# Optimization experiments

Measured on AMD Instinct MI355X. Metric: run time of the kernel, lower is better.

## Reference

```python
import jax, jax.numpy as jnp
import numpy as np

IN, OUT, HID = 1024, 1024, 2048
L = IN + OUT + HID
EPS = 1e-12  # F.normalize default eps


def _make_strength_matrix():
    fwd_s, bwd_s, lat_s, self_s = 1.0, 0.5, 0.3, 0.0
    i = np.arange(L)
    # torch: triu (incl diag) = forward, then tril (incl diag) = backward -> diag ends up backward here
    A = np.where(i[:, None] >= i[None, :], bwd_s, fwd_s).astype(np.float32)
    # lateral blocks (within input, within output, within hidden)
    A[0:IN, 0:IN] = lat_s
    A[IN:IN + OUT, IN:IN + OUT] = lat_s
    A[IN + OUT:L, IN + OUT:L] = lat_s
    A[i, i] = self_s
    return A


def setup_inputs() -> dict:
    key = jax.random.key(0)
    kx, ky, kw = jax.random.split(key, 3)
    B = 1024
    x = jax.random.normal(kx, (B, IN), dtype=jnp.float32)
    y = jax.random.normal(ky, (B, OUT), dtype=jnp.float32)
    W = jax.random.normal(kw, (L, L), dtype=jnp.float32) * 0.01
    idx = jnp.arange(L)
    W = W.at[idx, idx].set(0.0)  # fill_diagonal_(0) at init
    A = jnp.asarray(_make_strength_matrix())
    return {"x": x, "y": y, "W": W, "A": A, "n": 32}


def reference(x, y, W, A, n):
    # clamp_x=True, clamp_y=False, norm_hidden=True, average_window<=0
    B = x.shape[0]
    act0 = jnp.concatenate(
        [x, jnp.zeros_like(y), jnp.zeros((B, HID), dtype=x.dtype)], axis=1
    )  # [B, L]
    mw = W * A.T  # modified weights, loop-invariant

    def step(act, _):
        act = jax.nn.relu(act @ mw.T)          # linear(act, mw) + relu
        act = act.at[:, :IN].set(x)            # clamp_x
        hid = act[:, IN + OUT:]
        nrm = jnp.linalg.norm(hid, axis=1, keepdims=True)
        hid = hid / jnp.maximum(nrm, EPS)      # F.normalize p=2 dim=1
        act = act.at[:, IN + OUT:].set(hid)
        return act, None

    act, _ = jax.lax.scan(step, act0, None, length=n)
    return act
```

## Files before the change

kernel.cpp:

```cpp
#include <hip/hip_runtime.h>
#include <stdint.h>
#include <stddef.h>


#define L 4096
#define INX 1024
#define OUTX 1024
#define BATCH 1024
#define NCOL 3072
#define NITER 32

#define BM 128
#define BN 96
#define BK 64
#define SMEM_BYTES 86016

typedef float floatx4 __attribute__((ext_vector_type(4)));
typedef short bf16x8 __attribute__((ext_vector_type(8)));

__device__ __forceinline__ unsigned short f2bf(float f) {
  unsigned int u = __float_as_uint(f);
  u += 0x7FFF + ((u >> 16) & 1);
  return (unsigned short)(u >> 16);
}
__device__ __forceinline__ float bf2f(unsigned short h) {
  return __uint_as_float(((unsigned int)h) << 16);
}

__device__ __forceinline__ void load_lds_16B(const void* g, void* s) {
  __builtin_amdgcn_global_load_lds(
      (const __attribute__((address_space(1))) unsigned int*)g,
      (__attribute__((address_space(3))) unsigned int*)s, 16, 0, 0);
}

__global__ void prep_mwn(const float* __restrict__ W, unsigned short* __restrict__ mwn) {
  int idx = blockIdx.x * 256 + threadIdx.x;
  int i = idx >> 10;
  int j4 = (idx & 1023) << 2;
  const float4 w = *(const float4*)&W[(size_t)(INX + i) * L + j4];
  const int c = INX + i;
  const int rc = (c < 2048) ? 1 : 2;
  float wv[4] = {w.x, w.y, w.z, w.w};
  unsigned short o[4];
#pragma unroll
  for (int k = 0; k < 4; ++k) {
    int j = j4 + k;
    int rj = (j < 1024) ? 0 : ((j < 2048) ? 1 : 2);
    float a = (j == c) ? 0.0f : ((rj == rc) ? 0.3f : ((j >= c) ? 0.5f : 1.0f));
    o[k] = f2bf(wv[k] * a);
  }
  *(ushort4*)&mwn[(size_t)i * L + j4] = make_ushort4(o[0], o[1], o[2], o[3]);
}

__global__ void init_act(const float* __restrict__ x, unsigned short* __restrict__ actA) {
  int i = blockIdx.x * 256 + threadIdx.x;
  int col = i & (L - 1), row = i >> 12;
  actA[i] = (col < INX) ? f2bf(x[(size_t)row * INX + col]) : (unsigned short)0;
}

__device__ __forceinline__ void stage(unsigned short* As, unsigned short* Bs,
                                      const unsigned short* gA, const unsigned short* gB,
                                      int kb, int t) {
  const int srow = t >> 3, schunk = t & 7;
  const int o = srow * BK + schunk * 8;
  load_lds_16B(gA + kb, &As[o]);
  load_lds_16B(gA + (size_t)32 * L + kb, &As[o + 32 * BK]);
  load_lds_16B(gA + (size_t)64 * L + kb, &As[o + 64 * BK]);
  load_lds_16B(gA + (size_t)96 * L + kb, &As[o + 96 * BK]);
  load_lds_16B(gB + kb, &Bs[o]);
  load_lds_16B(gB + (size_t)32 * L + kb, &Bs[o + 32 * BK]);
  load_lds_16B(gB + (size_t)64 * L + kb, &Bs[o + 64 * BK]);
}

__device__ __forceinline__ void mfma_step(const unsigned short* As, const unsigned short* Bs,
                                          int wm, int wn, int l15, int quad,
                                          floatx4 acc[4][3]) {
#pragma unroll
  for (int kk = 0; kk < 2; ++kk) {
    bf16x8 af[4], bfr[3];
    const int c = kk * 4 + quad;
#pragma unroll
    for (int mt = 0; mt < 4; ++mt) {
      int r = wm + mt * 16 + l15;
      af[mt] = *(const bf16x8*)&As[r * BK + ((c ^ (r & 7)) * 8)];
    }
#pragma unroll
    for (int nt = 0; nt < 3; ++nt) {
      int r = wn + nt * 16 + l15;
      bfr[nt] = *(const bf16x8*)&Bs[r * BK + ((c ^ (r & 7)) * 8)];
    }
#pragma unroll
    for (int mt = 0; mt < 4; ++mt)
#pragma unroll
      for (int nt = 0; nt < 3; ++nt)
        acc[mt][nt] = __builtin_amdgcn_mfma_f32_16x16x32_bf16(af[mt], bfr[nt],
                                                              acc[mt][nt], 0, 0, 0);
  }
}

#define PSTEP(s, R, D, ACC)                                                       \
  do {                                                                            \
    if ((s) < NS - 1) asm volatile("s_waitcnt vmcnt(7)" ::: "memory");            \
    else              asm volatile("s_waitcnt vmcnt(0)" ::: "memory");            \
    asm volatile("s_barrier" ::: "memory");                                       \
    if ((s) + 2 < NS) stage(As##D, Bs##D, gA, gB, KB0 + ((s) + 2) * BK, t);       \
    mfma_step(As##R, Bs##R, wm, wn, l15, quad, ACC);                              \
  } while (0)

template<int MODE>
__global__ __launch_bounds__(256, 1) void gemm_k(
    const unsigned short* __restrict__ act,
    const unsigned short* __restrict__ mwn,
    unsigned short* __restrict__ actn,
    unsigned short* __restrict__ c0,
    const float* __restrict__ nsq_prev,
    float* __restrict__ nsq_next) {
  extern __shared__ unsigned short smem[];
  unsigned short* const As0 = smem;
  unsigned short* const As1 = smem + 8192;
  unsigned short* const As2 = smem + 16384;
  unsigned short* const Bs0 = smem + 24576;
  unsigned short* const Bs1 = smem + 30720;
  unsigned short* const Bs2 = smem + 36864;

  const int t = threadIdx.x;
  const int lane = t & 63;
  const int wave = t >> 6;
  const int wm = (wave >> 1) * 64;
  const int wn = (wave & 1) * 48;
  const int l15 = lane & 15;
  const int quad = lane >> 4;

  const int b = blockIdx.y * 32 + blockIdx.x;
  const int m_idx = b & 7;
  const int n_idx = b >> 3;
  const int m0 = m_idx * BM;
  const int n0 = n_idx * BN;

  const int srow = t >> 3;
  const int schunk = t & 7;
  const int gchunk = schunk ^ (srow & 7);
  const unsigned short* gA = act + (size_t)(m0 + srow) * L + gchunk * 8;
  const unsigned short* gB = mwn + (size_t)(n0 + srow) * L + gchunk * 8;

  const int KB0 = MODE ? INX : 0;
  constexpr int NS = MODE ? 48 : 16;

  floatx4 accA[4][3], accB[4][3];
#pragma unroll
  for (int i = 0; i < 4; ++i)
#pragma unroll
    for (int j = 0; j < 3; ++j) {
      accA[i][j] = (floatx4){0.f, 0.f, 0.f, 0.f};
      if (MODE) accB[i][j] = (floatx4){0.f, 0.f, 0.f, 0.f};
    }

  stage(As0, Bs0, gA, gB, KB0, t);
  stage(As1, Bs1, gA, gB, KB0 + BK, t);

  PSTEP(0, 0, 2, accA);  PSTEP(1, 1, 0, accA);  PSTEP(2, 2, 1, accA);
  PSTEP(3, 0, 2, accA);  PSTEP(4, 1, 0, accA);  PSTEP(5, 2, 1, accA);
  PSTEP(6, 0, 2, accA);  PSTEP(7, 1, 0, accA);  PSTEP(8, 2, 1, accA);
  PSTEP(9, 0, 2, accA);  PSTEP(10, 1, 0, accA); PSTEP(11, 2, 1, accA);
  PSTEP(12, 0, 2, accA); PSTEP(13, 1, 0, accA); PSTEP(14, 2, 1, accA);
  PSTEP(15, 0, 2, accA);
  if (MODE) {
    PSTEP(16, 1, 0, accB); PSTEP(17, 2, 1, accB); PSTEP(18, 0, 2, accB);
    PSTEP(19, 1, 0, accB); PSTEP(20, 2, 1, accB); PSTEP(21, 0, 2, accB);
    PSTEP(22, 1, 0, accB); PSTEP(23, 2, 1, accB); PSTEP(24, 0, 2, accB);
    PSTEP(25, 1, 0, accB); PSTEP(26, 2, 1, accB); PSTEP(27, 0, 2, accB);
    PSTEP(28, 1, 0, accB); PSTEP(29, 2, 1, accB); PSTEP(30, 0, 2, accB);
    PSTEP(31, 1, 0, accB); PSTEP(32, 2, 1, accB); PSTEP(33, 0, 2, accB);
    PSTEP(34, 1, 0, accB); PSTEP(35, 2, 1, accB); PSTEP(36, 0, 2, accB);
    PSTEP(37, 1, 0, accB); PSTEP(38, 2, 1, accB); PSTEP(39, 0, 2, accB);
    PSTEP(40, 1, 0, accB); PSTEP(41, 2, 1, accB); PSTEP(42, 0, 2, accB);
    PSTEP(43, 1, 0, accB); PSTEP(44, 2, 1, accB); PSTEP(45, 0, 2, accB);
    PSTEP(46, 1, 0, accB); PSTEP(47, 2, 1, accB);
  }

  if (MODE == 0) {
    alignas(16) unsigned short buf[48];
#pragma unroll
    for (int mt = 0; mt < 4; ++mt)
#pragma unroll
      for (int nt = 0; nt < 3; ++nt)
#pragma unroll
        for (int r = 0; r < 4; ++r)
          buf[mt * 12 + nt * 4 + r] = f2bf(accA[mt][nt][r]);
    unsigned short* p = c0 + ((size_t)b * 256 + t) * 48;
#pragma unroll
    for (int k = 0; k < 6; ++k)
      *(bf16x8*)&p[k * 8] = *(const bf16x8*)&buf[k * 8];
    return;
  }

  alignas(16) unsigned short c0s[48];
  {
    const unsigned short* p = c0 + ((size_t)b * 256 + t) * 48;
#pragma unroll
    for (int k = 0; k < 6; ++k)
      *(bf16x8*)&c0s[k * 8] = *(const bf16x8*)&p[k * 8];
  }

  float sm[4][4];
#pragma unroll
  for (int mt = 0; mt < 4; ++mt)
#pragma unroll
    for (int r = 0; r < 4; ++r) {
      const int gm = m0 + wm + mt * 16 + quad * 4 + r;
      sm[mt][r] = 1.0f / fmaxf(sqrtf(nsq_prev[gm]), 1e-12f);
    }

  const bool has_hid = (n0 + wn + 48) > OUTX;
#pragma unroll
  for (int mt = 0; mt < 4; ++mt) {
    float ss[4] = {0.f, 0.f, 0.f, 0.f};
#pragma unroll
    for (int nt = 0; nt < 3; ++nt) {
      const int gn = n0 + wn + nt * 16 + l15;
      const bool hid = gn >= OUTX;
#pragma unroll
      for (int r = 0; r < 4; ++r) {
        const int gm = m0 + wm + mt * 16 + quad * 4 + r;
        float v = bf2f(c0s[mt * 12 + nt * 4 + r]) + accA[mt][nt][r]
                  + sm[mt][r] * accB[mt][nt][r];
        v = fmaxf(v, 0.f);
        actn[(size_t)gm * L + INX + gn] = f2bf(v);
        if (hid) ss[r] += v * v;
      }
    }
    if (has_hid) {
#pragma unroll
      for (int r = 0; r < 4; ++r) {
        float sv = ss[r];
        sv += __shfl_xor(sv, 1);
        sv += __shfl_xor(sv, 2);
        sv += __shfl_xor(sv, 4);
        sv += __shfl_xor(sv, 8);
        if (l15 == 0)
          atomicAdd(&nsq_next[m0 + wm + mt * 16 + quad * 4 + r], sv);
      }
    }
  }
}

__global__ void finalize(const float* __restrict__ x, const unsigned short* __restrict__ act,
                         const float* __restrict__ nsq_fin, float* __restrict__ out) {
  int i = blockIdx.x * 256 + threadIdx.x;
  int col = i & (L - 1), row = i >> 12;
  float v;
  if (col < INX) {
    v = x[(size_t)row * INX + col];
  } else {
    v = bf2f(act[i]);
    if (col >= INX + OUTX) v *= 1.0f / fmaxf(sqrtf(nsq_fin[row]), 1e-12f);
  }
  out[i] = v;
}

extern "C" void kernel_launch(void* const* d_in, const int* in_sizes, int n_in,
                              void* d_out, int out_size, void* d_ws, size_t ws_size,
                              hipStream_t stream) {
  const float* x = (const float*)d_in[0];
  const float* W = (const float*)d_in[2];
  float* out = (float*)d_out;

  char* ws = (char*)d_ws;
  unsigned short* mwn  = (unsigned short*)(ws);
  unsigned short* actA = (unsigned short*)(ws + 25165824);
  unsigned short* actB = (unsigned short*)(ws + 33554432);
  unsigned short* c0   = (unsigned short*)(ws + 41943040);
  float* normsq        = (float*)(ws + 48234496);

  static bool attr_done = false;
  if (!attr_done) {
    (void)hipFuncSetAttribute(reinterpret_cast<const void*>(&gemm_k<0>),
                              hipFuncAttributeMaxDynamicSharedMemorySize, SMEM_BYTES);
    (void)hipFuncSetAttribute(reinterpret_cast<const void*>(&gemm_k<1>),
                              hipFuncAttributeMaxDynamicSharedMemorySize, SMEM_BYTES);
    attr_done = true;
  }

  hipMemsetAsync(normsq, 0, (NITER + 1) * BATCH * sizeof(float), stream);
  prep_mwn<<<(NCOL * (L / 4)) / 256, 256, 0, stream>>>(W, mwn);
  init_act<<<(BATCH * L) / 256, 256, 0, stream>>>(x, actA);

  gemm_k<0><<<dim3(32, 8), 256, SMEM_BYTES, stream>>>(actA, mwn, nullptr, c0,
                                                      nullptr, nullptr);

  unsigned short* cur = actA;
  unsigned short* nxt = actB;
  for (int it = 0; it < NITER; ++it) {
    gemm_k<1><<<dim3(32, 8), 256, SMEM_BYTES, stream>>>(
        cur, mwn, nxt, c0, normsq + it * BATCH, normsq + (it + 1) * BATCH);
    unsigned short* tmp = cur; cur = nxt; nxt = tmp;
  }
  finalize<<<(BATCH * L) / 256, 256, 0, stream>>>(x, cur, normsq + NITER * BATCH, out);
}
```

Measured before the change: 1.108 ms.

## Add register double-buffered fragments with four-stage LDS pipeline and remap block tiles

Expands the LDS ring from three to four stages and prefetches the next k-step's MFMA fragments into a second register set. Each step's LDS reads can then overlap with the current step's MFMAs, and global loads are issued three steps ahead. Block-to-tile mapping also changes so that consecutive blocks share the same M tile and spread across N tiles, which may change L2 reuse. The cost is more LDS (114 KB) and more VGPRs for the duplicated fragments, which could lead to spills or lower occupancy.

```diff
diff --git a/kernel.cpp b/kernel.cpp
--- a/kernel.cpp
+++ b/kernel.cpp
@@ -13,7 +13,7 @@
 #define BM 128
 #define BN 96
 #define BK 64
-#define SMEM_BYTES 86016
+#define SMEM_BYTES 114688
 
 typedef float floatx4 __attribute__((ext_vector_type(4)));
 typedef short bf16x8 __attribute__((ext_vector_type(8)));
@@ -72,39 +72,53 @@
   load_lds_16B(gB + (size_t)64 * L + kb, &Bs[o + 64 * BK]);
 }
 
-__device__ __forceinline__ void mfma_step(const unsigned short* As, const unsigned short* Bs,
-                                          int wm, int wn, int l15, int quad,
-                                          floatx4 acc[4][3]) {
+struct FragSet {
+  bf16x8 a[2][4];
+  bf16x8 b[2][3];
+};
+
+__device__ __forceinline__ void frag_read(FragSet& f, const unsigned short* As,
+                                          const unsigned short* Bs,
+                                          int wm, int wn, int l15, int quad) {
 #pragma unroll
   for (int kk = 0; kk < 2; ++kk) {
-    bf16x8 af[4], bfr[3];
     const int c = kk * 4 + quad;
 #pragma unroll
     for (int mt = 0; mt < 4; ++mt) {
       int r = wm + mt * 16 + l15;
-      af[mt] = *(const bf16x8*)&As[r * BK + ((c ^ (r & 7)) * 8)];
+      f.a[kk][mt] = *(const bf16x8*)&As[r * BK + ((c ^ (r & 7)) * 8)];
     }
 #pragma unroll
     for (int nt = 0; nt < 3; ++nt) {
       int r = wn + nt * 16 + l15;
-      bfr[nt] = *(const bf16x8*)&Bs[r * BK + ((c ^ (r & 7)) * 8)];
-    }
+      f.b[kk][nt] = *(const bf16x8*)&Bs[r * BK + ((c ^ (r & 7)) * 8)];
+    }
+  }
+}
+
+__device__ __forceinline__ void mfma_from(const FragSet& f, floatx4 acc[4][3]) {
+#pragma unroll
+  for (int kk = 0; kk < 2; ++kk)
 #pragma unroll
     for (int mt = 0; mt < 4; ++mt)
 #pragma unroll
       for (int nt = 0; nt < 3; ++nt)
-        acc[mt][nt] = __builtin_amdgcn_mfma_f32_16x16x32_bf16(af[mt], bfr[nt],
+        acc[mt][nt] = __builtin_amdgcn_mfma_f32_16x16x32_bf16(f.a[kk][mt], f.b[kk][nt],
                                                               acc[mt][nt], 0, 0, 0);
-  }
-}
-
-#define PSTEP(s, R, D, ACC)                                                       \
+}
+
+#define PSTEP(s, ACC)                                                             \
   do {                                                                            \
-    if ((s) < NS - 1) asm volatile("s_waitcnt vmcnt(7)" ::: "memory");            \
+    if ((s) + 2 < NS) asm volatile("s_waitcnt vmcnt(7)" ::: "memory");            \
     else              asm volatile("s_waitcnt vmcnt(0)" ::: "memory");            \
     asm volatile("s_barrier" ::: "memory");                                       \
-    if ((s) + 2 < NS) stage(As##D, Bs##D, gA, gB, KB0 + ((s) + 2) * BK, t);       \
-    mfma_step(As##R, Bs##R, wm, wn, l15, quad, ACC);                              \
+    if ((s) + 1 < NS)                                                             \
+      frag_read(fs[((s) + 1) & 1], AsP[((s) + 1) & 3], BsP[((s) + 1) & 3],        \
+                wm, wn, l15, quad);                                               \
+    if ((s) + 3 < NS)                                                             \
+      stage(AsP[((s) + 3) & 3], BsP[((s) + 3) & 3], gA, gB,                       \
+            KB0 + ((s) + 3) * BK, t);                                             \
+    mfma_from(fs[(s) & 1], ACC);                                                  \
   } while (0)
 
 template<int MODE>
@@ -116,12 +130,9 @@
     const float* __restrict__ nsq_prev,
     float* __restrict__ nsq_next) {
   extern __shared__ unsigned short smem[];
-  unsigned short* const As0 = smem;
-  unsigned short* const As1 = smem + 8192;
-  unsigned short* const As2 = smem + 16384;
-  unsigned short* const Bs0 = smem + 24576;
-  unsigned short* const Bs1 = smem + 30720;
-  unsigned short* const Bs2 = smem + 36864;
+  unsigned short* const AsP[4] = {smem, smem + 8192, smem + 16384, smem + 24576};
+  unsigned short* const BsP[4] = {smem + 32768, smem + 38912, smem + 45056,
+                                  smem + 51200};
 
   const int t = threadIdx.x;
   const int lane = t & 63;
@@ -132,8 +143,8 @@
   const int quad = lane >> 4;
 
   const int b = blockIdx.y * 32 + blockIdx.x;
-  const int m_idx = b & 7;
-  const int n_idx = b >> 3;
+  const int n_idx = (b & 7) * 4 + ((b >> 3) & 3);
+  const int m_idx = b >> 5;
   const int m0 = m_idx * BM;
   const int n0 = n_idx * BN;
 
@@ -155,27 +166,28 @@
       if (MODE) accB[i][j] = (floatx4){0.f, 0.f, 0.f, 0.f};
     }
 
-  stage(As0, Bs0, gA, gB, KB0, t);
-  stage(As1, Bs1, gA, gB, KB0 + BK, t);
-
-  PSTEP(0, 0, 2, accA);  PSTEP(1, 1, 0, accA);  PSTEP(2, 2, 1, accA);
-  PSTEP(3, 0, 2, accA);  PSTEP(4, 1, 0, accA);  PSTEP(5, 2, 1, accA);
-  PSTEP(6, 0, 2, accA);  PSTEP(7, 1, 0, accA);  PSTEP(8, 2, 1, accA);
-  PSTEP(9, 0, 2, accA);  PSTEP(10, 1, 0, accA); PSTEP(11, 2, 1, accA);
-  PSTEP(12, 0, 2, accA); PSTEP(13, 1, 0, accA); PSTEP(14, 2, 1, accA);
-  PSTEP(15, 0, 2, accA);
+  FragSet fs[2];
+
+  stage(AsP[0], BsP[0], gA, gB, KB0, t);
+  stage(AsP[1], BsP[1], gA, gB, KB0 + BK, t);
+  stage(AsP[2], BsP[2], gA, gB, KB0 + 2 * BK, t);
+  asm volatile("s_waitcnt vmcnt(14)" ::: "memory");
+  asm volatile("s_barrier" ::: "memory");
+  frag_read(fs[0], AsP[0], BsP[0], wm, wn, l15, quad);
+
+  PSTEP(0, accA);  PSTEP(1, accA);  PSTEP(2, accA);  PSTEP(3, accA);
+  PSTEP(4, accA);  PSTEP(5, accA);  PSTEP(6, accA);  PSTEP(7, accA);
+  PSTEP(8, accA);  PSTEP(9, accA);  PSTEP(10, accA); PSTEP(11, accA);
+  PSTEP(12, accA); PSTEP(13, accA); PSTEP(14, accA); PSTEP(15, accA);
   if (MODE) {
-    PSTEP(16, 1, 0, accB); PSTEP(17, 2, 1, accB); PSTEP(18, 0, 2, accB);
-    PSTEP(19, 1, 0, accB); PSTEP(20, 2, 1, accB); PSTEP(21, 0, 2, accB);
-    PSTEP(22, 1, 0, accB); PSTEP(23, 2, 1, accB); PSTEP(24, 0, 2, accB);
-    PSTEP(25, 1, 0, accB); PSTEP(26, 2, 1, accB); PSTEP(27, 0, 2, accB);
-    PSTEP(28, 1, 0, accB); PSTEP(29, 2, 1, accB); PSTEP(30, 0, 2, accB);
-    PSTEP(31, 1, 0, accB); PSTEP(32, 2, 1, accB); PSTEP(33, 0, 2, accB);
-    PSTEP(34, 1, 0, accB); PSTEP(35, 2, 1, accB); PSTEP(36, 0, 2, accB);
-    PSTEP(37, 1, 0, accB); PSTEP(38, 2, 1, accB); PSTEP(39, 0, 2, accB);
-    PSTEP(40, 1, 0, accB); PSTEP(41, 2, 1, accB); PSTEP(42, 0, 2, accB);
-    PSTEP(43, 1, 0, accB); PSTEP(44, 2, 1, accB); PSTEP(45, 0, 2, accB);
-    PSTEP(46, 1, 0, accB); PSTEP(47, 2, 1, accB);
+    PSTEP(16, accB); PSTEP(17, accB); PSTEP(18, accB); PSTEP(19, accB);
+    PSTEP(20, accB); PSTEP(21, accB); PSTEP(22, accB); PSTEP(23, accB);
+    PSTEP(24, accB); PSTEP(25, accB); PSTEP(26, accB); PSTEP(27, accB);
+    PSTEP(28, accB); PSTEP(29, accB); PSTEP(30, accB); PSTEP(31, accB);
+    PSTEP(32, accB); PSTEP(33, accB); PSTEP(34, accB); PSTEP(35, accB);
+    PSTEP(36, accB); PSTEP(37, accB); PSTEP(38, accB); PSTEP(39, accB);
+    PSTEP(40, accB); PSTEP(41, accB); PSTEP(42, accB); PSTEP(43, accB);
+    PSTEP(44, accB); PSTEP(45, accB); PSTEP(46, accB); PSTEP(47, accB);
   }
 
   if (MODE == 0) {
```

Result: no change. 1.109 ms (+0.1%).
